# Performance work log

Measured on AMD Instinct MI355X. Metric: run time of the kernel, lower is better.

The kernel has to match this reference:

```python
import jax, jax.numpy as jnp
import numpy as np

L, D, H, B, SX, SY, VS, VT = 6, 1024, 16, 4, 512, 512, 32000, 32000
DK = D // H
FF = 4 * D
EPS = 1e-3          # LayerNorm eps (added to std, not var)
SCALE_EMB = float(np.sqrt(D))
NEG = -1e30         # stands in for -inf; fully-masked rows are zeroed after softmax


def pos_encoding(length, d):
    # tensor2tensor-style sinusoid: [sin | cos] concatenated along channels
    nt = d // 2
    lti = np.log(1e4) / (nt - 1)
    inv = np.exp(np.arange(nt) * -lti)
    st = np.arange(length)[:, None] * inv[None, :]
    return jnp.asarray(np.concatenate([np.sin(st), np.cos(st)], axis=1), jnp.float32)


def layer_norm(z, a, b):
    # faithful to the torch module: uses unbiased std (ddof=1) and divides by (std + eps)
    mu = z.mean(-1, keepdims=True)
    sig = jnp.sqrt(((z - mu) ** 2).sum(-1, keepdims=True) / (z.shape[-1] - 1))
    return (z - mu) / (sig + EPS) * a + b


def mha(xq, xkv, wq, wk, wv, wo, mask):
    # xq: (b, lq, D), xkv: (b, lk, D); head-chunking of channel dim == reshape to (H, DK)
    b, lq, _ = xq.shape
    q = (xq @ wq.T).reshape(b, lq, H, DK)
    k = (xkv @ wk.T).reshape(b, -1, H, DK)
    v = (xkv @ wv.T).reshape(b, -1, H, DK)
    s = jnp.einsum('bqhd,bkhd->bhqk', q, k) * (1.0 / np.sqrt(DK))
    m = mask[:, None, :, :]
    s = jnp.where(m, s, NEG)
    att = jax.nn.softmax(s, axis=-1)
    att = att * m.any(-1, keepdims=True)  # replicates NaN->0 for fully masked rows
    c = jnp.einsum('bhqk,bkhd->bqhd', att, v).reshape(b, lq, D)
    return c @ wo.T


def setup_inputs():
    key = jax.random.key(0)
    ks = jax.random.split(key, 10)
    s = 0.02
    emb_x = (jax.random.normal(ks[0], (VS, D), jnp.float32) * s).at[0].set(0.0)  # padding_idx=0
    emb_y = (jax.random.normal(ks[1], (VT, D), jnp.float32) * s).at[0].set(0.0)
    return {
        'emb_x': emb_x, 'emb_y': emb_y,
        'enc_qkvo': jax.random.normal(ks[2], (L, 4, D, D), jnp.float32) * s,
        'enc_ln_s': jnp.ones((L, 2, D), jnp.float32), 'enc_ln_b': jnp.zeros((L, 2, D), jnp.float32),
        'enc_w1': jax.random.normal(ks[3], (L, FF, D), jnp.float32) * s, 'enc_b1': jnp.zeros((L, FF), jnp.float32),
        'enc_w2': jax.random.normal(ks[4], (L, D, FF), jnp.float32) * s, 'enc_b2': jnp.zeros((L, D), jnp.float32),
        'dec_qkvo': jax.random.normal(ks[5], (L, 8, D, D), jnp.float32) * s,
        'dec_ln_s': jnp.ones((L, 3, D), jnp.float32), 'dec_ln_b': jnp.zeros((L, 3, D), jnp.float32),
        'dec_w1': jax.random.normal(ks[6], (L, FF, D), jnp.float32) * s, 'dec_b1': jnp.zeros((L, FF), jnp.float32),
        'dec_w2': jax.random.normal(ks[7], (L, D, FF), jnp.float32) * s, 'dec_b2': jnp.zeros((L, D), jnp.float32),
        'x_block': jax.random.randint(ks[8], (B, SX), 0, VS),
        'y_block': jax.random.randint(ks[9], (B, SY), 0, VT),
    }


def reference(emb_x, emb_y, enc_qkvo, enc_ln_s, enc_ln_b, enc_w1, enc_b1, enc_w2, enc_b2,
              dec_qkvo, dec_ln_s, dec_ln_b, dec_w1, dec_b1, dec_w2, dec_b2, x_block, y_block):
    # internal layout (b, len, D); torch code uses (b, D, len) -- math is identical
    ex = emb_x[x_block] * SCALE_EMB + pos_encoding(SX, D)[None]
    ey = emb_y[y_block] * SCALE_EMB + pos_encoding(SY, D)[None]
    xv = x_block != 0
    yv = y_block != 0
    xx = xv[:, :, None] & xv[:, None, :]                                   # (B, qx, kx)
    xy = yv[:, :, None] & xv[:, None, :]                                   # (B, qy, kx)
    yy = (yv[:, :, None] & yv[:, None, :]) & jnp.tril(jnp.ones((SY, SY), bool))[None]
    e = ex
    for i in range(L):
        sub = mha(e, e, enc_qkvo[i, 0], enc_qkvo[i, 1], enc_qkvo[i, 2], enc_qkvo[i, 3], xx)
        e = layer_norm(e + sub, enc_ln_s[i, 0], enc_ln_b[i, 0])
        sub = jax.nn.relu(e @ enc_w1[i].T + enc_b1[i]) @ enc_w2[i].T + enc_b2[i]
        e = layer_norm(e + sub, enc_ln_s[i, 1], enc_ln_b[i, 1])
    z = e
    e = ey
    for i in range(L):
        sub = mha(e, e, dec_qkvo[i, 0], dec_qkvo[i, 1], dec_qkvo[i, 2], dec_qkvo[i, 3], yy)
        e = layer_norm(e + sub, dec_ln_s[i, 0], dec_ln_b[i, 0])
        sub = mha(e, z, dec_qkvo[i, 4], dec_qkvo[i, 5], dec_qkvo[i, 6], dec_qkvo[i, 7], xy)
        e = layer_norm(e + sub, dec_ln_s[i, 1], dec_ln_b[i, 1])
        sub = jax.nn.relu(e @ dec_w1[i].T + dec_b1[i]) @ dec_w2[i].T + dec_b2[i]
        e = layer_norm(e + sub, dec_ln_s[i, 2], dec_ln_b[i, 2])
    return e @ emb_y.T  # tied output projection -> (B, SY, VT)
```

## Files before the change

kernel.cpp:

```cpp
#include <hip/hip_runtime.h>

typedef unsigned short u16;
typedef float f32x4 __attribute__((ext_vector_type(4)));
typedef __bf16 bf16x8 __attribute__((ext_vector_type(8)));
typedef u16 u16x8 __attribute__((ext_vector_type(8)));

#define DEV __device__ __forceinline__

DEV u16 f2bf(float f) {
  unsigned u = __builtin_bit_cast(unsigned, f);
  u += 0x7fffu + ((u >> 16) & 1u);
  return (u16)(u >> 16);
}

DEV float wsum(float v) {
#pragma unroll
  for (int o = 32; o > 0; o >>= 1) v += __shfl_xor(v, o, 64);
  return v;
}
DEV float gmax16(float v) {
#pragma unroll
  for (int o = 8; o > 0; o >>= 1) v = fmaxf(v, __shfl_xor(v, o, 64));
  return v;
}
DEV float gsum16(float v) {
#pragma unroll
  for (int o = 8; o > 0; o >>= 1) v += __shfl_xor(v, o, 64);
  return v;
}

DEV void gld16(const void* g, void* l) {
  __builtin_amdgcn_global_load_lds((const __attribute__((address_space(1))) void*)g,
                                   (__attribute__((address_space(3))) void*)l, 16, 0, 0);
}

template <int N>
DEV void vwait() {
  if constexpr (N == 0) asm volatile("s_waitcnt vmcnt(0)" ::: "memory");
  else if constexpr (N == 3) asm volatile("s_waitcnt vmcnt(3)" ::: "memory");
  else if constexpr (N == 4) asm volatile("s_waitcnt vmcnt(4)" ::: "memory");
  else if constexpr (N == 6) asm volatile("s_waitcnt vmcnt(6)" ::: "memory");
  else asm volatile("s_waitcnt vmcnt(8)" ::: "memory");
}

DEV void remap_bxy(int& bx, int& by) {
  const int gx = gridDim.x, gy = gridDim.y;
  const int flat = blockIdx.y * gx + blockIdx.x;
  const int nwg = gx * gy;
  const int q = nwg >> 3, r = nwg & 7;
  const int xcd = flat & 7, li = flat >> 3;
  const int wg = (xcd < r ? xcd * (q + 1) : r * (q + 1) + (xcd - r) * q) + li;
  by = wg % gy;
  bx = wg / gy;
}

template <int BM, int BN, int MODE>
__global__ __launch_bounds__(256, 2) void gemm_k(
    const u16* __restrict__ A, const u16* __restrict__ B, int lda, int ldb, int K,
    float alpha, const float* __restrict__ bias, float* __restrict__ Cf, int ldc,
    u16* __restrict__ Cb, u16* __restrict__ qp, u16* __restrict__ kp,
    u16* __restrict__ vp, int n_off) {
  constexpr int FM = BM / 32, FN = BN / 32;
  constexpr int R = (BM + BN) >> 6;
  __shared__ u16 lds[4][(BM + BN) * 32];
  const int lane = threadIdx.x & 63, wid = threadIdx.x >> 6;
  const int wr = wid >> 1, wc = wid & 1;
  int bx, by;
  remap_bxy(bx, by);
  const u16* gA = A + (long)(by * BM) * lda;
  const u16* gB = B + (long)(bx * BN) * ldb;

  const f32x4 zero4 = {0.f, 0.f, 0.f, 0.f};
  f32x4 acc[FM][FN];
#pragma unroll
  for (int m = 0; m < FM; ++m)
#pragma unroll
    for (int n = 0; n < FN; ++n) acc[m][n] = zero4;

  auto stage = [&](int t) {
    const int kb = t << 5;
    u16* lbase = &lds[t & 3][0];
#pragma unroll
    for (int rd = 0; rd < R; ++rd) {
      const int c = rd * 256 + threadIdx.x;
      const int r = c >> 2;
      const int sg = (c & 3) ^ ((r >> 1) & 3);
      const u16* g = (r < BM) ? (gA + (long)r * lda + kb + (sg << 3))
                              : (gB + (long)(r - BM) * ldb + kb + (sg << 3));
      gld16(g, lbase + (c << 3));
    }
  };

  const int KT = K >> 5;
  stage(0);
  stage(1);
  stage(2);
  for (int t = 0; t < KT; ++t) {
    const int rem = KT - 1 - t;
    if (rem >= 2) vwait<2 * R>();
    else if (rem == 1) vwait<R>();
    else vwait<0>();
    __builtin_amdgcn_s_barrier();
    __builtin_amdgcn_sched_barrier(0);
    if (t + 3 < KT) stage(t + 3);
    const u16* lA = &lds[t & 3][0];
    const u16* lB = lA + (BM << 5);
    bf16x8 af[FM], bv[FN];
#pragma unroll
    for (int m = 0; m < FM; ++m) {
      int r = wr * (BM / 2) + m * 16 + (lane & 15);
      int sg = (lane >> 4) ^ ((r >> 1) & 3);
      af[m] = *(const bf16x8*)(lA + (r << 5) + (sg << 3));
    }
#pragma unroll
    for (int n = 0; n < FN; ++n) {
      int c = wc * (BN / 2) + n * 16 + (lane & 15);
      int sg = (lane >> 4) ^ ((c >> 1) & 3);
      bv[n] = *(const bf16x8*)(lB + (c << 5) + (sg << 3));
    }
#pragma unroll
    for (int m = 0; m < FM; ++m)
#pragma unroll
      for (int n = 0; n < FN; ++n)
        acc[m][n] = __builtin_amdgcn_mfma_f32_16x16x32_bf16(af[m], bv[n], acc[m][n], 0, 0, 0);
    __builtin_amdgcn_sched_barrier(0);
  }

  const int rb = by * BM + wr * (BM / 2) + ((lane >> 4) << 2);
  const int cb = bx * BN + wc * (BN / 2) + (lane & 15);
  if constexpr (MODE == 2) {
    const bool isV = (bx * BN + n_off) >= 2048;
    if (isV) {
      __syncthreads();
      u16* T = (u16*)&lds[0][0];
      constexpr int TS = BM + 8;
#pragma unroll
      for (int m = 0; m < FM; ++m)
#pragma unroll
        for (int n = 0; n < FN; ++n) {
          int cl = wc * (BN / 2) + n * 16 + (lane & 15);
#pragma unroll
          for (int j = 0; j < 4; ++j) {
            int rl = wr * (BM / 2) + m * 16 + ((lane >> 4) << 2) + j;
            T[cl * TS + rl] = f2bf(acc[m][n][j]);
          }
        }
      __syncthreads();
      const int vcb = bx * BN + n_off - 2048;
      const int b = (by * BM) >> 9, s0 = (by * BM) & 511;
#pragma unroll
      for (int p = 0; p < BM * BN / 2048; ++p) {
        int idx = p * 2048 + threadIdx.x * 8;
        int dl = idx / BM, sl = idx & (BM - 1);
        u16x8 o;
#pragma unroll
        for (int e = 0; e < 8; ++e) o[e] = T[dl * TS + sl + e];
        int vc = vcb + dl;
        *(u16x8*)(vp + (((long)b * 16 + (vc >> 6)) * 64 + (vc & 63)) * 512 + s0 + sl) = o;
      }
    } else {
#pragma unroll
      for (int m = 0; m < FM; ++m)
#pragma unroll
        for (int n = 0; n < FN; ++n)
#pragma unroll
          for (int j = 0; j < 4; ++j) {
            const int row = rb + m * 16 + j;
            const int np = cb + n * 16 + n_off;
            const int sel = np >> 10, dim = np & 1023;
            long base = (((long)(row >> 9) * 16 + (dim >> 6)) * 512 + (row & 511)) * 64 + (dim & 63);
            u16 val = f2bf(acc[m][n][j]);
            if (sel == 0) qp[base] = val;
            else kp[base] = val;
          }
    }
  } else {
#pragma unroll
    for (int m = 0; m < FM; ++m)
#pragma unroll
      for (int n = 0; n < FN; ++n)
#pragma unroll
        for (int j = 0; j < 4; ++j) {
          const int row = rb + m * 16 + j;
          const int col = cb + n * 16;
          float v = acc[m][n][j];
          if constexpr (MODE == 0) {
            float r = v * alpha;
            if (bias) r += bias[col];
            Cf[(long)row * ldc + col] = r;
          } else {
            Cb[(long)row * ldc + col] = f2bf(fmaxf(v + bias[col], 0.f));
          }
        }
  }
}

template <int CAUSAL>
__global__ __launch_bounds__(256, 2) void fattn_k(
    const u16* __restrict__ Qg, const u16* __restrict__ Kg, const u16* __restrict__ Vtg,
    const int* __restrict__ qids, const int* __restrict__ kids, u16* __restrict__ ctx) {
  __shared__ u16 Qs[128 * 64];
  __shared__ u16 Ks[2][64 * 64];
  __shared__ u16 Vs[2][64 * 64];
  __shared__ u16 Ps[4][32 * 64];
  const int lane = threadIdx.x & 63, wid = threadIdx.x >> 6;
  const int qt = blockIdx.x, bh = blockIdx.y, b = bh >> 4, h = bh & 15;
  const int q0 = qt << 7;
  const u16* Qbase = Qg + ((long)bh * 512 + q0) * 64;
  const u16* Kbase = Kg + (long)bh * 512 * 64;
  const u16* Vbase = Vtg + (long)bh * 64 * 512;
  const int r8 = lane >> 3, sl = lane & 7;

#pragma unroll
  for (int c0 = 0; c0 < 16; c0 += 4) {
    int c = c0 + wid;
    int r = (c << 3) + r8;
    gld16(Qbase + (long)r * 64 + ((sl ^ (r & 7)) << 3), &Qs[c << 9]);
  }

  auto stageKV = [&](int buf, int kt) {
#pragma unroll
    for (int c0 = 0; c0 < 16; c0 += 4) {
      int c = c0 + wid;
      if (c < 8) {
        int r = (c << 3) + r8;
        gld16(Kbase + (long)(kt * 64 + r) * 64 + ((sl ^ (r & 7)) << 3), &Ks[buf][c << 9]);
      } else {
        int r = ((c - 8) << 3) + r8;
        gld16(Vbase + (long)r * 512 + kt * 64 + ((sl ^ (r & 7)) << 3), &Vs[buf][(c - 8) << 9]);
      }
    }
  };

  const int NKT = CAUSAL ? ((q0 >> 6) + 2) : 8;
  stageKV(0, 0);
  __syncthreads();

  const f32x4 z4 = {0.f, 0.f, 0.f, 0.f};
  f32x4 oacc[2][4];
  float mrun[2][4], lrun[2][4];
  bool qv[2][4];
#pragma unroll
  for (int m = 0; m < 2; ++m)
#pragma unroll
    for (int j = 0; j < 4; ++j) {
      mrun[m][j] = -3e38f;
      lrun[m][j] = 0.f;
      int qg = q0 + wid * 32 + m * 16 + ((lane >> 4) << 2) + j;
      qv[m][j] = qids[(b << 9) + qg] != 0;
#pragma unroll
      for (int nd = 0; nd < 4; ++nd) oacc[m][nd] = z4;
    }

  int cur = 0;
  for (int kt = 0; kt < NKT; ++kt) {
    if (kt + 1 < NKT) stageKV(cur ^ 1, kt + 1);
    f32x4 s[2][4];
#pragma unroll
    for (int m = 0; m < 2; ++m)
#pragma unroll
      for (int n = 0; n < 4; ++n) s[m][n] = z4;
    __builtin_amdgcn_s_setprio(1);
#pragma unroll
    for (int kk = 0; kk < 2; ++kk) {
      bf16x8 aq[2], bk[4];
#pragma unroll
      for (int m = 0; m < 2; ++m) {
        int r = wid * 32 + m * 16 + (lane & 15);
        int slot = ((kk << 2) | (lane >> 4)) ^ (r & 7);
        aq[m] = *(const bf16x8*)&Qs[(r << 6) + (slot << 3)];
      }
#pragma unroll
      for (int n = 0; n < 4; ++n) {
        int c = n * 16 + (lane & 15);
        int slot = ((kk << 2) | (lane >> 4)) ^ (c & 7);
        bk[n] = *(const bf16x8*)&Ks[cur][(c << 6) + (slot << 3)];
      }
#pragma unroll
      for (int m = 0; m < 2; ++m)
#pragma unroll
        for (int n = 0; n < 4; ++n)
          s[m][n] = __builtin_amdgcn_mfma_f32_16x16x32_bf16(aq[m], bk[n], s[m][n], 0, 0, 0);
    }
    __builtin_amdgcn_s_setprio(0);
    bool kvld[4];
#pragma unroll
    for (int n = 0; n < 4; ++n)
      kvld[n] = kids[(b << 9) + (kt << 6) + (n << 4) + (lane & 15)] != 0;
    float mx[2][4];
#pragma unroll
    for (int m = 0; m < 2; ++m)
#pragma unroll
      for (int j = 0; j < 4; ++j) {
        mx[m][j] = -3e38f;
        int qg = q0 + wid * 32 + m * 16 + ((lane >> 4) << 2) + j;
#pragma unroll
        for (int n = 0; n < 4; ++n) {
          int colg = (kt << 6) + (n << 4) + (lane & 15);
          bool ok = qv[m][j] && kvld[n] && (!CAUSAL || colg <= qg);
          float sv = ok ? s[m][n][j] * 0.125f : -3e38f;
          s[m][n][j] = sv;
          mx[m][j] = fmaxf(mx[m][j], sv);
        }
        mx[m][j] = gmax16(mx[m][j]);
      }
#pragma unroll
    for (int m = 0; m < 2; ++m)
#pragma unroll
      for (int j = 0; j < 4; ++j) {
        float mn = fmaxf(mrun[m][j], mx[m][j]);
        float f = __expf(mrun[m][j] - mn);
        mrun[m][j] = mn;
        float ps = 0.f;
#pragma unroll
        for (int n = 0; n < 4; ++n) {
          float sv = s[m][n][j];
          float p = (sv > -1e37f) ? __expf(sv - mn) : 0.f;
          s[m][n][j] = p;
          ps += p;
        }
        ps = gsum16(ps);
        lrun[m][j] = lrun[m][j] * f + ps;
#pragma unroll
        for (int nd = 0; nd < 4; ++nd) oacc[m][nd][j] *= f;
      }
#pragma unroll
    for (int m = 0; m < 2; ++m)
#pragma unroll
      for (int n = 0; n < 4; ++n)
#pragma unroll
        for (int j = 0; j < 4; ++j) {
          int rl = (m << 4) + ((lane >> 4) << 2) + j;
          int slot = ((n << 1) | ((lane >> 3) & 1)) ^ (rl & 7);
          Ps[wid][(rl << 6) + (slot << 3) + (lane & 7)] = f2bf(s[m][n][j]);
        }
    __builtin_amdgcn_s_setprio(1);
#pragma unroll
    for (int kk = 0; kk < 2; ++kk) {
      bf16x8 pa[2], vv[4];
#pragma unroll
      for (int m = 0; m < 2; ++m) {
        int r = (m << 4) + (lane & 15);
        int slot = ((kk << 2) | (lane >> 4)) ^ (r & 7);
        pa[m] = *(const bf16x8*)&Ps[wid][(r << 6) + (slot << 3)];
      }
#pragma unroll
      for (int nd = 0; nd < 4; ++nd) {
        int rv = (nd << 4) + (lane & 15);
        int slot = ((kk << 2) | (lane >> 4)) ^ (rv & 7);
        vv[nd] = *(const bf16x8*)&Vs[cur][(rv << 6) + (slot << 3)];
      }
#pragma unroll
      for (int m = 0; m < 2; ++m)
#pragma unroll
        for (int nd = 0; nd < 4; ++nd)
          oacc[m][nd] = __builtin_amdgcn_mfma_f32_16x16x32_bf16(pa[m], vv[nd], oacc[m][nd], 0, 0, 0);
    }
    __builtin_amdgcn_s_setprio(0);
    __syncthreads();
    cur ^= 1;
  }
#pragma unroll
  for (int m = 0; m < 2; ++m)
#pragma unroll
    for (int j = 0; j < 4; ++j) {
      float inv = (lrun[m][j] > 0.f) ? 1.0f / lrun[m][j] : 0.f;
      int qg = q0 + wid * 32 + m * 16 + ((lane >> 4) << 2) + j;
      long rowb = (((long)(b << 9) + qg) * 16 + h) * 64;
#pragma unroll
      for (int nd = 0; nd < 4; ++nd) {
        int d = (nd << 4) + (lane & 15);
        ctx[rowb + d] = f2bf(oacc[m][nd][j] * inv);
      }
    }
}

__global__ __launch_bounds__(256) void embed_k(const int* __restrict__ ids,
                                               const float* __restrict__ emb,
                                               float* __restrict__ xo, u16* __restrict__ bfo) {
  const int tok = blockIdx.x, t = threadIdx.x;
  const int s = tok & 511;
  const long id = ids[tok];
  const int d = t * 4;
  float4 ev = *(const float4*)(emb + id * 1024 + d);
  float o[4] = {ev.x * 32.f, ev.y * 32.f, ev.z * 32.f, ev.w * 32.f};
#pragma unroll
  for (int j = 0; j < 4; ++j) {
    int dd = d + j, di = dd & 511;
    float ang = (float)s * expf(-(float)di * 0.0180241494559220821f);
    o[j] += (dd < 512) ? sinf(ang) : cosf(ang);
  }
  *(float4*)(xo + (long)tok * 1024 + d) = make_float4(o[0], o[1], o[2], o[3]);
  ushort4 ob = {f2bf(o[0]), f2bf(o[1]), f2bf(o[2]), f2bf(o[3])};
  *(ushort4*)(bfo + (long)tok * 1024 + d) = ob;
}

__global__ __launch_bounds__(256) void ln_k(const float* __restrict__ x,
                                            const float* __restrict__ sub,
                                            const float* __restrict__ gam,
                                            const float* __restrict__ bet,
                                            float* __restrict__ xo, u16* __restrict__ bfo) {
  __shared__ float red[8];
  const int row = blockIdx.x, t = threadIdx.x;
  const float4 xv = *(const float4*)(x + (long)row * 1024 + t * 4);
  const float4 sv = *(const float4*)(sub + (long)row * 1024 + t * 4);
  float v0 = xv.x + sv.x, v1 = xv.y + sv.y, v2 = xv.z + sv.z, v3 = xv.w + sv.w;
  float sm = wsum(v0 + v1 + v2 + v3);
  if ((t & 63) == 0) red[t >> 6] = sm;
  __syncthreads();
  const float mu = (red[0] + red[1] + red[2] + red[3]) * (1.0f / 1024.0f);
  const float d0 = v0 - mu, d1 = v1 - mu, d2 = v2 - mu, d3 = v3 - mu;
  float ss = wsum(d0 * d0 + d1 * d1 + d2 * d2 + d3 * d3);
  if ((t & 63) == 0) red[4 + (t >> 6)] = ss;
  __syncthreads();
  const float sig = sqrtf((red[4] + red[5] + red[6] + red[7]) * (1.0f / 1023.0f));
  const float inv = 1.0f / (sig + 0.001f);
  const float4 g4 = *(const float4*)(gam + t * 4);
  const float4 b4 = *(const float4*)(bet + t * 4);
  const float o0 = d0 * inv * g4.x + b4.x, o1 = d1 * inv * g4.y + b4.y;
  const float o2 = d2 * inv * g4.z + b4.z, o3 = d3 * inv * g4.w + b4.w;
  *(float4*)(xo + (long)row * 1024 + t * 4) = make_float4(o0, o1, o2, o3);
  ushort4 ob = {f2bf(o0), f2bf(o1), f2bf(o2), f2bf(o3)};
  *(ushort4*)(bfo + (long)row * 1024 + t * 4) = ob;
}

__global__ void cvt_k(const float* __restrict__ src, u16* __restrict__ dst, int n4) {
  for (int i = blockIdx.x * 256 + threadIdx.x; i < n4; i += gridDim.x * 256) {
    float4 v = ((const float4*)src)[i];
    ushort4 o = {f2bf(v.x), f2bf(v.y), f2bf(v.z), f2bf(v.w)};
    ((ushort4*)dst)[i] = o;
  }
}

__global__ void cvt3_k(const float* __restrict__ s0, int n0, const float* __restrict__ s1,
                       int n1, const float* __restrict__ s2, int n2, u16* __restrict__ dst) {
  const int tot = n0 + n1 + n2;
  for (int i = blockIdx.x * 256 + threadIdx.x; i < tot; i += gridDim.x * 256) {
    const float* s;
    int j;
    if (i < n0) { s = s0; j = i; }
    else if (i < n0 + n1) { s = s1; j = i - n0; }
    else { s = s2; j = i - n0 - n1; }
    float4 v = ((const float4*)s)[j];
    ushort4 o = {f2bf(v.x), f2bf(v.y), f2bf(v.z), f2bf(v.w)};
    ((ushort4*)dst)[i] = o;
  }
}

extern "C" void kernel_launch(void* const* d_in, const int* in_sizes, int n_in, void* d_out,
                              int out_size, void* d_ws, size_t ws_size, hipStream_t stream) {
  (void)in_sizes; (void)n_in; (void)out_size;
  const float* emb_x = (const float*)d_in[0];
  const float* emb_y = (const float*)d_in[1];
  const float* enc_qkvo = (const float*)d_in[2];
  const float* enc_ln_s = (const float*)d_in[3];
  const float* enc_ln_b = (const float*)d_in[4];
  const float* enc_w1 = (const float*)d_in[5];
  const float* enc_b1 = (const float*)d_in[6];
  const float* enc_w2 = (const float*)d_in[7];
  const float* enc_b2 = (const float*)d_in[8];
  const float* dec_qkvo = (const float*)d_in[9];
  const float* dec_ln_s = (const float*)d_in[10];
  const float* dec_ln_b = (const float*)d_in[11];
  const float* dec_w1 = (const float*)d_in[12];
  const float* dec_b1 = (const float*)d_in[13];
  const float* dec_w2 = (const float*)d_in[14];
  const float* dec_b2 = (const float*)d_in[15];
  const int* x_block = (const int*)d_in[16];
  const int* y_block = (const int*)d_in[17];

  const long TOK = 2048, Dm = 1024, M1 = 1048576;
  char* p = (char*)d_ws;
  auto alloc = [&](long bytes) { char* r = p; p += (bytes + 255) & ~255L; return r; };
  float* e32 = (float*)alloc(TOK * Dm * 4);
  float* sub = (float*)alloc(TOK * Dm * 4);
  u16* ebf = (u16*)alloc(TOK * Dm * 2);
  u16* zbf = (u16*)alloc(TOK * Dm * 2);
  u16* qb = (u16*)alloc(TOK * Dm * 2);
  u16* kb = (u16*)alloc(TOK * Dm * 2);
  u16* vtb = (u16*)alloc(TOK * Dm * 2);
  u16* ctx = (u16*)alloc(TOK * Dm * 2);
  u16* hbuf = (u16*)alloc(TOK * 4096 * 2);
  u16* wbuf = (u16*)alloc(16L * M1 * 2);
  u16* embyb = (u16*)alloc(32000L * 1024 * 2);
  if ((size_t)(p - (char*)d_ws) > ws_size) return;

  auto gemmF = [&](const u16* A, const u16* Bw, int M, int N, int K, int lda, int ldb,
                   float alpha, const float* bias, float* C, int ldc) {
    if (N % 128 == 0 && N > 1024) {
      dim3 g(N / 128, M / 128);
      gemm_k<128, 128, 0><<<g, 256, 0, stream>>>(A, Bw, lda, ldb, K, alpha, bias, C, ldc,
                                                 nullptr, nullptr, nullptr, nullptr, 0);
    } else {
      dim3 g(N / 64, M / 128);
      gemm_k<128, 64, 0><<<g, 256, 0, stream>>>(A, Bw, lda, ldb, K, alpha, bias, C, ldc,
                                                nullptr, nullptr, nullptr, nullptr, 0);
    }
  };
  auto gemmRelu = [&](const u16* A, const u16* Bw, const float* bias, u16* C) {
    dim3 g(32, 16);
    gemm_k<128, 128, 1><<<g, 256, 0, stream>>>(A, Bw, 1024, 1024, 1024, 1.f, bias, nullptr,
                                               4096, C, nullptr, nullptr, nullptr, 0);
  };
  auto gemmQKV = [&](const u16* A, const u16* Bw, int N, int n_off) {
    if (N >= 2048) {
      dim3 g(N / 128, 16);
      gemm_k<128, 128, 2><<<g, 256, 0, stream>>>(A, Bw, 1024, 1024, 1024, 1.f, nullptr,
                                                 nullptr, 0, nullptr, qb, kb, vtb, n_off);
    } else {
      dim3 g(N / 64, 16);
      gemm_k<128, 64, 2><<<g, 256, 0, stream>>>(A, Bw, 1024, 1024, 1024, 1.f, nullptr,
                                                nullptr, 0, nullptr, qb, kb, vtb, n_off);
    }
  };
  auto attn = [&](const int* qids, const int* kids, int causal) {
    if (causal)
      fattn_k<1><<<dim3(4, 64), 256, 0, stream>>>(qb, kb, vtb, qids, kids, ctx);
    else
      fattn_k<0><<<dim3(4, 64), 256, 0, stream>>>(qb, kb, vtb, qids, kids, ctx);
  };
  auto lnorm = [&](const float* g, const float* b) {
    ln_k<<<2048, 256, 0, stream>>>(e32, sub, g, b, e32, ebf);
  };

  cvt_k<<<2048, 256, 0, stream>>>(emb_y, embyb, 32000 * 1024 / 4);

  embed_k<<<2048, 256, 0, stream>>>(x_block, emb_x, e32, ebf);
  for (int i = 0; i < 6; ++i) {
    cvt3_k<<<2048, 256, 0, stream>>>(enc_qkvo + (long)i * 4 * M1, (int)M1,
                                     enc_w1 + (long)i * 4 * M1, (int)M1,
                                     enc_w2 + (long)i * 4 * M1, (int)M1, wbuf);
    gemmQKV(ebf, wbuf, 3072, 0);
    attn(x_block, x_block, 0);
    gemmF(ctx, wbuf + 3L * M1, 2048, 1024, 1024, 1024, 1024, 1.f, nullptr, sub, 1024);
    lnorm(enc_ln_s + (i * 2 + 0) * 1024, enc_ln_b + (i * 2 + 0) * 1024);
    gemmRelu(ebf, wbuf + 4L * M1, enc_b1 + i * 4096, hbuf);
    gemmF(hbuf, wbuf + 8L * M1, 2048, 1024, 4096, 4096, 4096, 1.f, enc_b2 + i * 1024, sub, 1024);
    lnorm(enc_ln_s + (i * 2 + 1) * 1024, enc_ln_b + (i * 2 + 1) * 1024);
  }
  hipMemcpyAsync(zbf, ebf, TOK * Dm * 2, hipMemcpyDeviceToDevice, stream);

  embed_k<<<2048, 256, 0, stream>>>(y_block, emb_y, e32, ebf);
  for (int i = 0; i < 6; ++i) {
    cvt3_k<<<2048, 256, 0, stream>>>(dec_qkvo + (long)i * 8 * M1, (int)(2 * M1),
                                     dec_w1 + (long)i * 4 * M1, (int)M1,
                                     dec_w2 + (long)i * 4 * M1, (int)M1, wbuf);
    gemmQKV(ebf, wbuf, 3072, 0);
    attn(y_block, y_block, 1);
    gemmF(ctx, wbuf + 3L * M1, 2048, 1024, 1024, 1024, 1024, 1.f, nullptr, sub, 1024);
    lnorm(dec_ln_s + (i * 3 + 0) * 1024, dec_ln_b + (i * 3 + 0) * 1024);
    gemmQKV(ebf, wbuf + 4L * M1, 1024, 0);
    gemmQKV(zbf, wbuf + 5L * M1, 2048, 1024);
    attn(y_block, x_block, 0);
    gemmF(ctx, wbuf + 7L * M1, 2048, 1024, 1024, 1024, 1024, 1.f, nullptr, sub, 1024);
    lnorm(dec_ln_s + (i * 3 + 1) * 1024, dec_ln_b + (i * 3 + 1) * 1024);
    gemmRelu(ebf, wbuf + 8L * M1, dec_b1 + i * 4096, hbuf);
    gemmF(hbuf, wbuf + 12L * M1, 2048, 1024, 4096, 4096, 4096, 1.f, dec_b2 + i * 1024, sub, 1024);
    lnorm(dec_ln_s + (i * 3 + 2) * 1024, dec_ln_b + (i * 3 + 2) * 1024);
  }
  gemmF(ebf, embyb, 2048, 32000, 1024, 1024, 1024, 1.f, nullptr, (float*)d_out, 32000);
}
```

Baseline: 2.547 ms.

## Add 256x256 ping-pong GEMM for vocab projection and retile generic GEMM K-loop

Adds a dedicated 512-thread GEMM kernel with 256x256 tiles, double-buffered LDS and staged quarter-tile loads interleaved with MFMA phases and priority hints. It is used for the large tied output projection to 32000 logits. The generic GEMM also moves from a 4-stage, K=32 pipeline to a 2-buffer, K=64 pipeline with an XOR swizzle and a full __syncthreads per step. The large kernel aims at more data reuse and better load/compute overlap, but the simpler generic pipeline may expose more load latency.

Measured after the change: 2.563 ms. No clear change (+0.6%).

```diff
diff --git a/kernel.cpp b/kernel.cpp
--- a/kernel.cpp
+++ b/kernel.cpp
@@ -37,10 +37,9 @@
 template <int N>
 DEV void vwait() {
   if constexpr (N == 0) asm volatile("s_waitcnt vmcnt(0)" ::: "memory");
-  else if constexpr (N == 3) asm volatile("s_waitcnt vmcnt(3)" ::: "memory");
+  else if constexpr (N == 2) asm volatile("s_waitcnt vmcnt(2)" ::: "memory");
   else if constexpr (N == 4) asm volatile("s_waitcnt vmcnt(4)" ::: "memory");
-  else if constexpr (N == 6) asm volatile("s_waitcnt vmcnt(6)" ::: "memory");
-  else asm volatile("s_waitcnt vmcnt(8)" ::: "memory");
+  else asm volatile("s_waitcnt vmcnt(6)" ::: "memory");
 }
 
 DEV void remap_bxy(int& bx, int& by) {
@@ -61,8 +60,8 @@
     u16* __restrict__ Cb, u16* __restrict__ qp, u16* __restrict__ kp,
     u16* __restrict__ vp, int n_off) {
   constexpr int FM = BM / 32, FN = BN / 32;
-  constexpr int R = (BM + BN) >> 6;
-  __shared__ u16 lds[4][(BM + BN) * 32];
+  constexpr int CHA = BM / 8, CHT = (BM + BN) / 8;
+  __shared__ u16 lds[2][(BM + BN) * 64];
   const int lane = threadIdx.x & 63, wid = threadIdx.x >> 6;
   const int wr = wid >> 1, wc = wid & 1;
   int bx, by;
@@ -77,53 +76,57 @@
 #pragma unroll
     for (int n = 0; n < FN; ++n) acc[m][n] = zero4;
 
-  auto stage = [&](int t) {
-    const int kb = t << 5;
-    u16* lbase = &lds[t & 3][0];
-#pragma unroll
-    for (int rd = 0; rd < R; ++rd) {
-      const int c = rd * 256 + threadIdx.x;
-      const int r = c >> 2;
-      const int sg = (c & 3) ^ ((r >> 1) & 3);
-      const u16* g = (r < BM) ? (gA + (long)r * lda + kb + (sg << 3))
-                              : (gB + (long)(r - BM) * ldb + kb + (sg << 3));
-      gld16(g, lbase + (c << 3));
+  const int r8 = lane >> 3, sl = lane & 7;
+
+  auto stage = [&](int buf, int kt) {
+    const int kb = kt << 6;
+#pragma unroll
+    for (int c0 = 0; c0 < CHT; c0 += 4) {
+      const int c = c0 + wid;
+      u16* l = &lds[buf][c << 9];
+      const u16* g;
+      if (c < CHA) {
+        int r = (c << 3) + r8;
+        g = gA + (long)r * lda + kb + ((sl ^ (r & 7)) << 3);
+      } else {
+        int r = ((c - CHA) << 3) + r8;
+        g = gB + (long)r * ldb + kb + ((sl ^ (r & 7)) << 3);
+      }
+      gld16(g, l);
     }
   };
 
-  const int KT = K >> 5;
-  stage(0);
-  stage(1);
-  stage(2);
-  for (int t = 0; t < KT; ++t) {
-    const int rem = KT - 1 - t;
-    if (rem >= 2) vwait<2 * R>();
-    else if (rem == 1) vwait<R>();
-    else vwait<0>();
-    __builtin_amdgcn_s_barrier();
-    __builtin_amdgcn_sched_barrier(0);
-    if (t + 3 < KT) stage(t + 3);
-    const u16* lA = &lds[t & 3][0];
-    const u16* lB = lA + (BM << 5);
-    bf16x8 af[FM], bv[FN];
-#pragma unroll
-    for (int m = 0; m < FM; ++m) {
-      int r = wr * (BM / 2) + m * 16 + (lane & 15);
-      int sg = (lane >> 4) ^ ((r >> 1) & 3);
-      af[m] = *(const bf16x8*)(lA + (r << 5) + (sg << 3));
-    }
-#pragma unroll
-    for (int n = 0; n < FN; ++n) {
-      int c = wc * (BN / 2) + n * 16 + (lane & 15);
-      int sg = (lane >> 4) ^ ((c >> 1) & 3);
-      bv[n] = *(const bf16x8*)(lB + (c << 5) + (sg << 3));
-    }
-#pragma unroll
-    for (int m = 0; m < FM; ++m)
-#pragma unroll
-      for (int n = 0; n < FN; ++n)
-        acc[m][n] = __builtin_amdgcn_mfma_f32_16x16x32_bf16(af[m], bv[n], acc[m][n], 0, 0, 0);
-    __builtin_amdgcn_sched_barrier(0);
+  const int KT = K >> 6;
+  stage(0, 0);
+  __syncthreads();
+  int cur = 0;
+  for (int kt = 0; kt < KT; ++kt) {
+    if (kt + 1 < KT) stage(cur ^ 1, kt + 1);
+    const u16* lA = &lds[cur][0];
+    const u16* lB = &lds[cur][BM << 6];
+#pragma unroll
+    for (int kk = 0; kk < 2; ++kk) {
+      bf16x8 af[FM], bv[FN];
+#pragma unroll
+      for (int m = 0; m < FM; ++m) {
+        int r = wr * (BM / 2) + m * 16 + (lane & 15);
+        int slot = ((kk << 2) | (lane >> 4)) ^ (r & 7);
+        af[m] = *(const bf16x8*)(lA + (r << 6) + (slot << 3));
+      }
+#pragma unroll
+      for (int n = 0; n < FN; ++n) {
+        int r = wc * (BN / 2) + n * 16 + (lane & 15);
+        int slot = ((kk << 2) | (lane >> 4)) ^ (r & 7);
+        bv[n] = *(const bf16x8*)(lB + (r << 6) + (slot << 3));
+      }
+#pragma unroll
+      for (int m = 0; m < FM; ++m)
+#pragma unroll
+        for (int n = 0; n < FN; ++n)
+          acc[m][n] = __builtin_amdgcn_mfma_f32_16x16x32_bf16(af[m], bv[n], acc[m][n], 0, 0, 0);
+    }
+    __syncthreads();
+    cur ^= 1;
   }
 
   const int rb = by * BM + wr * (BM / 2) + ((lane >> 4) << 2);
@@ -151,12 +154,12 @@
 #pragma unroll
       for (int p = 0; p < BM * BN / 2048; ++p) {
         int idx = p * 2048 + threadIdx.x * 8;
-        int dl = idx / BM, sl = idx & (BM - 1);
+        int dl = idx / BM, slx = idx & (BM - 1);
         u16x8 o;
 #pragma unroll
-        for (int e = 0; e < 8; ++e) o[e] = T[dl * TS + sl + e];
+        for (int e = 0; e < 8; ++e) o[e] = T[dl * TS + slx + e];
         int vc = vcb + dl;
-        *(u16x8*)(vp + (((long)b * 16 + (vc >> 6)) * 64 + (vc & 63)) * 512 + s0 + sl) = o;
+        *(u16x8*)(vp + (((long)b * 16 + (vc >> 6)) * 64 + (vc & 63)) * 512 + s0 + slx) = o;
       }
     } else {
 #pragma unroll
@@ -193,6 +196,160 @@
           }
         }
   }
+}
+
+__global__ __launch_bounds__(512, 1) void gemm256_k(
+    const u16* __restrict__ A, const u16* __restrict__ B, int lda, int ldb, int K,
+    float* __restrict__ Cf, int ldc) {
+  __shared__ u16 As[2][256 * 64];
+  __shared__ u16 Bs[2][256 * 64];
+  const int lane = threadIdx.x & 63, wid = threadIdx.x >> 6;
+  const int wr = wid >> 2, wc = wid & 3;
+  int bx, by;
+  remap_bxy(bx, by);
+  const u16* gA = A + (long)(by * 256) * lda;
+  const u16* gB = B + (long)(bx * 256) * ldb;
+
+  const f32x4 z4 = {0.f, 0.f, 0.f, 0.f};
+  f32x4 acc[8][4];
+#pragma unroll
+  for (int m = 0; m < 8; ++m)
+#pragma unroll
+    for (int n = 0; n < 4; ++n) acc[m][n] = z4;
+
+  const int ssl = lane & 7;
+
+  auto stageH = [&](int t, int h) {
+    const int kb = t << 6;
+    const int buf = t & 1;
+    const bool isA = (h == 0) || (h == 3);
+    u16* ldsb = isA ? &As[buf][0] : &Bs[buf][0];
+    const u16* gsrc = isA ? gA : gB;
+    const int ld = isA ? lda : ldb;
+    const int rbase = (h >= 2) ? 128 : 0;
+#pragma unroll
+    for (int rr = 0; rr < 2; ++rr) {
+      const int r0 = rbase + rr * 64 + (wid << 3);
+      const int r = r0 + (lane >> 3);
+      gld16(gsrc + (long)r * ld + kb + ((ssl ^ (r & 7)) << 3), ldsb + (r0 << 6));
+    }
+  };
+
+  const int KT = K >> 6;
+  stageH(0, 0);
+  stageH(0, 1);
+  stageH(0, 2);
+  stageH(0, 3);
+
+  for (int t = 0; t < KT; ++t) {
+    const int buf = t & 1;
+    const bool more = (t + 1 < KT);
+    const u16* lA = &As[buf][0];
+    const u16* lB = &Bs[buf][0];
+    bf16x8 af[4][2], bvl[2][2], bvh[2][2];
+
+    vwait<4>();
+    __builtin_amdgcn_s_barrier();
+    __builtin_amdgcn_sched_barrier(0);
+#pragma unroll
+    for (int m = 0; m < 4; ++m)
+#pragma unroll
+      for (int kk = 0; kk < 2; ++kk) {
+        int r = wr * 64 + m * 16 + (lane & 15);
+        int sg = ((kk << 2) | (lane >> 4)) ^ (r & 7);
+        af[m][kk] = *(const bf16x8*)(lA + (r << 6) + (sg << 3));
+      }
+#pragma unroll
+    for (int n = 0; n < 2; ++n)
+#pragma unroll
+      for (int kk = 0; kk < 2; ++kk) {
+        int c = wc * 32 + n * 16 + (lane & 15);
+        int sg = ((kk << 2) | (lane >> 4)) ^ (c & 7);
+        bvl[n][kk] = *(const bf16x8*)(lB + (c << 6) + (sg << 3));
+      }
+    if (more) stageH(t + 1, 0);
+    __builtin_amdgcn_s_setprio(1);
+#pragma unroll
+    for (int kk = 0; kk < 2; ++kk)
+#pragma unroll
+      for (int m = 0; m < 4; ++m)
+#pragma unroll
+        for (int n = 0; n < 2; ++n)
+          acc[m][n] = __builtin_amdgcn_mfma_f32_16x16x32_bf16(af[m][kk], bvl[n][kk], acc[m][n], 0, 0, 0);
+    __builtin_amdgcn_s_setprio(0);
+
+    if (more) vwait<4>();
+    else vwait<2>();
+    __builtin_amdgcn_s_barrier();
+    __builtin_amdgcn_sched_barrier(0);
+#pragma unroll
+    for (int n = 0; n < 2; ++n)
+#pragma unroll
+      for (int kk = 0; kk < 2; ++kk) {
+        int c = 128 + wc * 32 + n * 16 + (lane & 15);
+        int sg = ((kk << 2) | (lane >> 4)) ^ (c & 7);
+        bvh[n][kk] = *(const bf16x8*)(lB + (c << 6) + (sg << 3));
+      }
+    if (more) stageH(t + 1, 1);
+    __builtin_amdgcn_s_setprio(1);
+#pragma unroll
+    for (int kk = 0; kk < 2; ++kk)
+#pragma unroll
+      for (int m = 0; m < 4; ++m)
+#pragma unroll
+        for (int n = 0; n < 2; ++n)
+          acc[m][2 + n] = __builtin_amdgcn_mfma_f32_16x16x32_bf16(af[m][kk], bvh[n][kk], acc[m][2 + n], 0, 0, 0);
+    __builtin_amdgcn_s_setprio(0);
+
+    if (more) vwait<4>();
+    else vwait<0>();
+    __builtin_amdgcn_s_barrier();
+    __builtin_amdgcn_sched_barrier(0);
+#pragma unroll
+    for (int m = 0; m < 4; ++m)
+#pragma unroll
+      for (int kk = 0; kk < 2; ++kk) {
+        int r = 128 + wr * 64 + m * 16 + (lane & 15);
+        int sg = ((kk << 2) | (lane >> 4)) ^ (r & 7);
+        af[m][kk] = *(const bf16x8*)(lA + (r << 6) + (sg << 3));
+      }
+    if (more) stageH(t + 1, 2);
+    __builtin_amdgcn_s_setprio(1);
+#pragma unroll
+    for (int kk = 0; kk < 2; ++kk)
+#pragma unroll
+      for (int m = 0; m < 4; ++m)
+#pragma unroll
+        for (int n = 0; n < 2; ++n)
+          acc[4 + m][2 + n] = __builtin_amdgcn_mfma_f32_16x16x32_bf16(af[m][kk], bvh[n][kk], acc[4 + m][2 + n], 0, 0, 0);
+    __builtin_amdgcn_s_setprio(0);
+
+    __builtin_amdgcn_s_barrier();
+    __builtin_amdgcn_sched_barrier(0);
+    if (more) stageH(t + 1, 3);
+    __builtin_amdgcn_s_setprio(1);
+#pragma unroll
+    for (int kk = 0; kk < 2; ++kk)
+#pragma unroll
+      for (int m = 0; m < 4; ++m)
+#pragma unroll
+        for (int n = 0; n < 2; ++n)
+          acc[4 + m][n] = __builtin_amdgcn_mfma_f32_16x16x32_bf16(af[m][kk], bvl[n][kk], acc[4 + m][n], 0, 0, 0);
+    __builtin_amdgcn_s_setprio(0);
+  }
+
+  const int rb = by * 256 + wr * 64 + ((lane >> 4) << 2);
+  const int cb = bx * 256 + wc * 32 + (lane & 15);
+#pragma unroll
+  for (int mi = 0; mi < 8; ++mi)
+#pragma unroll
+    for (int ni = 0; ni < 4; ++ni)
+#pragma unroll
+      for (int j = 0; j < 4; ++j) {
+        int row = rb + (mi & 3) * 16 + ((mi >> 2) << 7) + j;
+        int col = cb + (ni & 1) * 16 + ((ni >> 1) << 7);
+        Cf[(long)row * ldc + col] = acc[mi][ni][j];
+      }
 }
 
 template <int CAUSAL>
@@ -558,5 +715,6 @@
     gemmF(hbuf, wbuf + 12L * M1, 2048, 1024, 4096, 4096, 4096, 1.f, dec_b2 + i * 1024, sub, 1024);
     lnorm(dec_ln_s + (i * 3 + 2) * 1024, dec_ln_b + (i * 3 + 2) * 1024);
   }
-  gemmF(ebf, embyb, 2048, 32000, 1024, 1024, 1024, 1.f, nullptr, (float*)d_out, 32000);
-}
+  gemm256_k<<<dim3(125, 8), 512, 0, stream>>>(ebf, embyb, 1024, 1024, 1024,
+                                              (float*)d_out, 32000);
+}
```
